# Optimization experiments

Measured on AMD Instinct MI355X. Metric: run time of the kernel, lower is better.

Reference implementation:

```python
import jax, jax.numpy as jnp
import numpy as np

B, N, DIM, H = 8, 2048, 64, 8  # per-head dim == DIM (module convention: inner_dim = dim * n_heads)


def setup_inputs() -> dict:
    key = jax.random.key(0)
    k1, k2, k3 = jax.random.split(key, 3)
    x = jax.random.normal(k1, (B, N, DIM), dtype=jnp.float32)
    W_qkv = jax.random.normal(k2, (DIM, 3 * H * DIM), dtype=jnp.float32) * (DIM ** -0.5)
    W_out = jax.random.normal(k3, (H * DIM, DIM), dtype=jnp.float32) * ((H * DIM) ** -0.5)
    b_out = jnp.zeros((DIM,), dtype=jnp.float32)
    return {"x": x, "W_qkv": W_qkv, "W_out": W_out, "b_out": b_out}


def reference(x, W_qkv, W_out, b_out):
    b, n, d = x.shape
    h = W_qkv.shape[1] // (3 * d)
    qkv = x @ W_qkv                                   # [b, n, 3*h*d]
    q, k, v = jnp.split(qkv, 3, axis=-1)              # each [b, n, h*d]
    def to_heads(t):
        return t.reshape(b, n, h, d).transpose(0, 2, 1, 3)  # [b, h, n, d]
    q, k, v = map(to_heads, (q, k, v))
    scale = d ** -0.5
    dot = jnp.einsum('bhid,bhjd->bhij', q, k) * scale  # [b, h, n, n]
    A = jax.nn.softmax(dot, axis=-1)
    z = jnp.einsum('bhij,bhjd->bhid', A, v)            # [b, h, n, d]
    z = z.transpose(0, 2, 1, 3).reshape(b, n, h * d)   # [b, n, h*d]
    return z @ W_out + b_out                           # [b, n, d]
```

## Files before the change

### kernel.cpp

```cpp
#include <hip/hip_runtime.h>
#include <math.h>

#define BB 8
#define NN 2048
#define DD 64
#define HH 8
#define BH (BB*HH)
#define HD (HH*DD)
#define NROWS (BB*NN)
#define QKV_COLS (3*HD)

typedef __bf16 bf16_8 __attribute__((ext_vector_type(8)));
typedef __bf16 bf16_4 __attribute__((ext_vector_type(4)));
typedef float  f32_16 __attribute__((ext_vector_type(16)));
typedef float  f32_4  __attribute__((ext_vector_type(4)));
typedef int    i32_2  __attribute__((ext_vector_type(2)));

__device__ __forceinline__ unsigned pack_bf16(float a, float b) {
  union { __bf16 h[2]; unsigned u; } t;
  t.h[0] = (__bf16)a; t.h[1] = (__bf16)b;
  return t.u;
}

__device__ __forceinline__ float fast_exp2(float x) {
#if __has_builtin(__builtin_amdgcn_exp2f)
  return __builtin_amdgcn_exp2f(x);
#else
  return __expf(x * 0.69314718056f);
#endif
}

__global__ __launch_bounds__(256) void wtrans_kernel(
    const float* __restrict__ Wqkv, const float* __restrict__ Wout,
    __bf16* __restrict__ Wtq, __bf16* __restrict__ Wto) {
  int idx = blockIdx.x * 256 + threadIdx.x;
  if (idx < 64 * QKV_COLS) {
    int k = idx / QKV_COLS, col = idx % QKV_COLS;
    float v = Wqkv[idx];
    if (col < HD) v *= 0.125f * 1.44269504088896f;
    Wtq[col * 64 + k] = (__bf16)v;
    (void)k;
  } else {
    int j = idx - 64 * QKV_COLS;
    int k = j >> 6, col = j & 63;
    Wto[col * 512 + k] = (__bf16)Wout[j];
  }
}

__global__ __launch_bounds__(256) void qkv_kernel(
    const float* __restrict__ x, const __bf16* __restrict__ Wtq,
    __bf16* __restrict__ Q, __bf16* __restrict__ K, __bf16* __restrict__ Vt) {
  __shared__ __bf16 T[4][64][34];
  const int lane = threadIdx.x & 63;
  const int wave = threadIdx.x >> 6;
  const int l31  = lane & 31, lhi = lane >> 5;
  const int cg   = blockIdx.x;
  const int row0 = blockIdx.y * 128 + wave * 32;

  const float* xr = x + (size_t)(row0 + l31) * 64 + lhi * 8;
  bf16_8 af[4];
#pragma unroll
  for (int s = 0; s < 4; s++) {
    f32_4 a0 = *(const f32_4*)(xr + s * 16);
    f32_4 a1 = *(const f32_4*)(xr + s * 16 + 4);
#pragma unroll
    for (int j = 0; j < 4; j++) { af[s][j] = (__bf16)a0[j]; af[s][4 + j] = (__bf16)a1[j]; }
  }

  f32_16 C0, C1;
#pragma unroll
  for (int i = 0; i < 16; i++) { C0[i] = 0.f; C1[i] = 0.f; }

  const __bf16* wb = Wtq + (size_t)cg * 64 * 64 + lhi * 8;
#pragma unroll
  for (int s = 0; s < 4; s++) {
    bf16_8 b0 = *(const bf16_8*)(wb + (size_t)l31 * 64 + s * 16);
    bf16_8 b1 = *(const bf16_8*)(wb + (size_t)(32 + l31) * 64 + s * 16);
    C0 = __builtin_amdgcn_mfma_f32_32x32x16_bf16(af[s], b0, C0, 0, 0, 0);
    C1 = __builtin_amdgcn_mfma_f32_32x32x16_bf16(af[s], b1, C1, 0, 0, 0);
  }

  const int col0  = cg * 64;
  const int which = col0 >> 9;
  const int h     = (col0 >> 6) & 7;
  const int b     = row0 >> 11;
  const int n0l   = row0 & 2047;

  if (which < 2) {
    __bf16* dst = (which == 0) ? Q : K;
#pragma unroll
    for (int r = 0; r < 16; r++) {
      int nl = (r & 3) + 8 * (r >> 2) + 4 * lhi;
      size_t base = (((size_t)(b * HH + h) * NN) + n0l + nl) * DD;
      dst[base + l31]      = (__bf16)C0[r];
      dst[base + 32 + l31] = (__bf16)C1[r];
    }
  } else {
    __bf16 (*Tw)[34] = T[wave];
#pragma unroll
    for (int r = 0; r < 16; r++) {
      int nl = (r & 3) + 8 * (r >> 2) + 4 * lhi;
      Tw[l31][nl]      = (__bf16)C0[r];
      Tw[32 + l31][nl] = (__bf16)C1[r];
    }
    __bf16* dst = Vt + (((size_t)(b * HH + h) * DD) + lane) * NN + n0l;
#pragma unroll
    for (int j = 0; j < 4; j++) {
      *(bf16_8*)(dst + j * 8) = *(const bf16_8*)(&Tw[lane][j * 8]);
    }
  }
}

__global__ __launch_bounds__(256, 3) void attn_kernel(
    const __bf16* __restrict__ Q, const __bf16* __restrict__ K,
    const __bf16* __restrict__ Vt, __bf16* __restrict__ z) {
  __shared__ __bf16 Ks[128 * 72];
  __shared__ __bf16 Vs[64 * 136];

  const int tid  = threadIdx.x;
  const int wave = tid >> 6;
  const int lane = tid & 63;
  const int l31  = lane & 31;
  const int lhi  = lane >> 5;
  const int xl   = lane ^ 32;
  const int bh   = blockIdx.x >> 4;
  const int q0   = (blockIdx.x & 15) * 128 + wave * 32;

  const __bf16* Qbase = Q + ((size_t)bh * NN + q0 + l31) * DD + lhi * 8;
  bf16_8 qf[4];
#pragma unroll
  for (int s = 0; s < 4; s++) qf[s] = *(const bf16_8*)(Qbase + s * 16);

  f32_16 O0, O1;
#pragma unroll
  for (int i = 0; i < 16; i++) { O0[i] = 0.f; O1[i] = 0.f; }
  float ls0 = 0.f, ls1 = 0.f;

  const __bf16* Kb = K  + (size_t)bh * NN * DD;
  const __bf16* Vb = Vt + (size_t)bh * DD * NN;

  const int krow = tid >> 3, kcol = (tid & 7) * 8;
  const int vrow = tid >> 4, vcol = (tid & 15) * 8;
  const __bf16* kgl = Kb + krow * 64 + kcol;
  const __bf16* vgl = Vb + (size_t)vrow * NN + vcol;
  __bf16* klds = &Ks[krow * 72 + kcol];
  __bf16* vlds = &Vs[vrow * 136 + vcol];

  bf16_8 gk[4], gv[4];
#pragma unroll
  for (int i = 0; i < 4; i++) {
    gk[i] = *(const bf16_8*)(kgl + i * 32 * 64);
    gv[i] = *(const bf16_8*)(vgl + i * 16 * NN);
  }

  for (int kt = 0; kt < NN; kt += 128) {
    __syncthreads();
#pragma unroll
    for (int i = 0; i < 4; i++) {
      *(bf16_8*)(klds + i * 32 * 72)  = gk[i];
      *(bf16_8*)(vlds + i * 16 * 136) = gv[i];
    }
    __syncthreads();
    if (kt + 128 < NN) {
#pragma unroll
      for (int i = 0; i < 4; i++) {
        gk[i] = *(const bf16_8*)(kgl + (kt + 128) * 64 + i * 32 * 64);
        gv[i] = *(const bf16_8*)(vgl + (kt + 128) + i * 16 * NN);
      }
    }

#pragma unroll
    for (int hf = 0; hf < 2; hf++) {
      f32_16 S0, S1;
#pragma unroll
      for (int i = 0; i < 16; i++) { S0[i] = 0.f; S1[i] = 0.f; }
#pragma unroll
      for (int s = 0; s < 4; s++) {
        bf16_8 kb0 = *(const bf16_8*)(&Ks[(hf * 64 + l31) * 72 + s * 16 + lhi * 8]);
        bf16_8 kb1 = *(const bf16_8*)(&Ks[(hf * 64 + 32 + l31) * 72 + s * 16 + lhi * 8]);
        S0 = __builtin_amdgcn_mfma_f32_32x32x16_bf16(kb0, qf[s], S0, 0, 0, 0);
        S1 = __builtin_amdgcn_mfma_f32_32x32x16_bf16(kb1, qf[s], S1, 0, 0, 0);
      }

      unsigned pk[16];
#pragma unroll
      for (int t = 0; t < 8; t++) {
        float a = fast_exp2(S0[2 * t]), b = fast_exp2(S0[2 * t + 1]);
        float c = fast_exp2(S1[2 * t]), d = fast_exp2(S1[2 * t + 1]);
        ls0 += a + b;
        ls1 += c + d;
        pk[t]     = pack_bf16(a, b);
        pk[8 + t] = pack_bf16(c, d);
      }

#pragma unroll
      for (int g = 0; g < 4; g++) {
        const int base = (g >> 1) * 8 + (g & 1) * 4;
        int a0 = (int)pk[base + 0], a1 = (int)pk[base + 1];
        int a2 = (int)pk[base + 2], a3 = (int)pk[base + 3];
        union { unsigned u[4]; bf16_8 v; } F;
#if __has_builtin(__builtin_amdgcn_permlane32_swap)
        i32_2 r02 = __builtin_amdgcn_permlane32_swap(a0, a2, false, false);
        i32_2 r13 = __builtin_amdgcn_permlane32_swap(a1, a3, false, false);
        F.u[0] = (unsigned)r02.x; F.u[2] = (unsigned)r02.y;
        F.u[1] = (unsigned)r13.x; F.u[3] = (unsigned)r13.y;
#else
        unsigned w0 = (unsigned)__shfl(a0, xl, 64);
        unsigned w1 = (unsigned)__shfl(a1, xl, 64);
        unsigned w2 = (unsigned)__shfl(a2, xl, 64);
        unsigned w3 = (unsigned)__shfl(a3, xl, 64);
        F.u[0] = lhi ? w2 : (unsigned)a0;
        F.u[1] = lhi ? w3 : (unsigned)a1;
        F.u[2] = lhi ? (unsigned)a2 : w0;
        F.u[3] = lhi ? (unsigned)a3 : w1;
#endif
        bf16_8 va0 = *(const bf16_8*)(&Vs[l31 * 136 + hf * 64 + g * 16 + lhi * 8]);
        bf16_8 va1 = *(const bf16_8*)(&Vs[(32 + l31) * 136 + hf * 64 + g * 16 + lhi * 8]);
        O0 = __builtin_amdgcn_mfma_f32_32x32x16_bf16(va0, F.v, O0, 0, 0, 0);
        O1 = __builtin_amdgcn_mfma_f32_32x32x16_bf16(va1, F.v, O1, 0, 0, 0);
      }
    }
  }

  float lsum = ls0 + ls1;
  lsum += __shfl_xor(lsum, 32, 64);
  const float inv = 1.f / lsum;

  __syncthreads();
  __bf16* ow = Ks + wave * (32 * 72);
#pragma unroll
  for (int g = 0; g < 4; g++) {
    bf16_4 p0, p1;
#pragma unroll
    for (int i = 0; i < 4; i++) {
      p0[i] = (__bf16)(O0[4 * g + i] * inv);
      p1[i] = (__bf16)(O1[4 * g + i] * inv);
    }
    const int d0 = 8 * g + 4 * lhi;
    *(bf16_4*)(ow + l31 * 72 + d0)      = p0;
    *(bf16_4*)(ow + l31 * 72 + 32 + d0) = p1;
  }
  const int b = bh >> 3, h = bh & 7;
  const int qr = lane >> 1, c0 = (lane & 1) * 32;
  __bf16* zp = z + ((size_t)b * NN + q0 + qr) * HD + h * DD + c0;
#pragma unroll
  for (int j = 0; j < 4; j++) {
    *(bf16_8*)(zp + 8 * j) = *(const bf16_8*)(ow + qr * 72 + c0 + 8 * j);
  }
}

__global__ __launch_bounds__(256) void out_proj_kernel(
    const __bf16* __restrict__ z, const __bf16* __restrict__ Wto,
    const float* __restrict__ bout, float* __restrict__ out) {
  __shared__ float red[2][64][36];
  const int tid  = threadIdx.x;
  const int wave = tid >> 6, lane = tid & 63;
  const int rt   = wave >> 1, kh = wave & 1;
  const int l31  = lane & 31, lhi = lane >> 5;
  const int row0 = blockIdx.x * 64 + rt * 32;

  const __bf16* zr = z   + (size_t)(row0 + l31) * HD + kh * 256 + lhi * 8;
  const __bf16* w0 = Wto + (size_t)l31 * HD        + kh * 256 + lhi * 8;
  const __bf16* w1 = Wto + (size_t)(32 + l31) * HD + kh * 256 + lhi * 8;

  f32_16 C0, C1;
#pragma unroll
  for (int i = 0; i < 16; i++) { C0[i] = 0.f; C1[i] = 0.f; }

#pragma unroll
  for (int s = 0; s < 16; s++) {
    bf16_8 a  = *(const bf16_8*)(zr + s * 16);
    bf16_8 b0 = *(const bf16_8*)(w0 + s * 16);
    bf16_8 b1 = *(const bf16_8*)(w1 + s * 16);
    C0 = __builtin_amdgcn_mfma_f32_32x32x16_bf16(a, b0, C0, 0, 0, 0);
    C1 = __builtin_amdgcn_mfma_f32_32x32x16_bf16(a, b1, C1, 0, 0, 0);
  }

  float* rw = &red[rt][lane][0];
  if (kh) {
#pragma unroll
    for (int r = 0; r < 16; r++) { rw[r] = C0[r]; rw[16 + r] = C1[r]; }
  }
  __syncthreads();
  if (!kh) {
    const float bi0 = bout[l31], bi1 = bout[32 + l31];
#pragma unroll
    for (int r = 0; r < 16; r++) {
      int n = row0 + (r & 3) + 8 * (r >> 2) + 4 * lhi;
      out[(size_t)n * 64 + l31]      = C0[r] + rw[r]      + bi0;
      out[(size_t)n * 64 + 32 + l31] = C1[r] + rw[16 + r] + bi1;
    }
  }
}

extern "C" void kernel_launch(void* const* d_in, const int* in_sizes, int n_in,
                              void* d_out, int out_size, void* d_ws, size_t ws_size,
                              hipStream_t stream) {
  const float* x    = (const float*)d_in[0];
  const float* Wqkv = (const float*)d_in[1];
  const float* Wout = (const float*)d_in[2];
  const float* bout = (const float*)d_in[3];
  float* out = (float*)d_out;

  const size_t buf_elems = (size_t)BB * HH * NN * DD;
  __bf16* Qw  = (__bf16*)d_ws;
  __bf16* Kw  = Qw  + buf_elems;
  __bf16* Vtw = Kw  + buf_elems;
  __bf16* zw  = Vtw + buf_elems;
  __bf16* Wtq = zw  + buf_elems;
  __bf16* Wto = Wtq + (size_t)QKV_COLS * 64;

  wtrans_kernel<<<512, 256, 0, stream>>>(Wqkv, Wout, Wtq, Wto);
  qkv_kernel<<<dim3(QKV_COLS / 64, NROWS / 128), 256, 0, stream>>>(x, Wtq, Qw, Kw, Vtw);
  attn_kernel<<<BH * (NN / 128), 256, 0, stream>>>(Qw, Kw, Vtw, zw);
  out_proj_kernel<<<NROWS / 64, 256, 0, stream>>>(zw, Wto, bout, out);
}
```

Before: 192.9 us.

## Fold weight prep into QKV kernel, widen attention blocks, split out-proj K four ways

Removes the separate weight-transpose kernel. The QKV kernel now reads the fp32 W_qkv directly with on-the-fly scaling and bf16 conversion, and an extra grid row packs W_out into an MFMA-friendly layout. The attention kernel moves to 512-thread blocks covering 256 queries, so each K/V tile staged in LDS is shared by twice as many waves. The output projection uses 32-row blocks with a four-way K split reduced through LDS. The cost is strided uncoalesced weight loads inside the QKV GEMM, and out_proj's read of the packed W_out now depends on writes made by an extra block row of the previous kernel on the same stream.

```diff
diff --git a/kernel.cpp b/kernel.cpp
--- a/kernel.cpp
+++ b/kernel.cpp
@@ -16,6 +16,8 @@
 typedef float  f32_4  __attribute__((ext_vector_type(4)));
 typedef int    i32_2  __attribute__((ext_vector_type(2)));
 
+#define QSCALE 0.180336880111f
+
 __device__ __forceinline__ unsigned pack_bf16(float a, float b) {
   union { __bf16 h[2]; unsigned u; } t;
   t.h[0] = (__bf16)a; t.h[1] = (__bf16)b;
@@ -30,27 +32,46 @@
 #endif
 }
 
-__global__ __launch_bounds__(256) void wtrans_kernel(
-    const float* __restrict__ Wqkv, const float* __restrict__ Wout,
-    __bf16* __restrict__ Wtq, __bf16* __restrict__ Wto) {
-  int idx = blockIdx.x * 256 + threadIdx.x;
-  if (idx < 64 * QKV_COLS) {
-    int k = idx / QKV_COLS, col = idx % QKV_COLS;
-    float v = Wqkv[idx];
-    if (col < HD) v *= 0.125f * 1.44269504088896f;
-    Wtq[col * 64 + k] = (__bf16)v;
-    (void)k;
-  } else {
-    int j = idx - 64 * QKV_COLS;
-    int k = j >> 6, col = j & 63;
-    Wto[col * 512 + k] = (__bf16)Wout[j];
-  }
+__device__ __forceinline__ bf16_8 half_swap(unsigned a0, unsigned a1,
+                                            unsigned a2, unsigned a3,
+                                            int lhi, int xl) {
+  union { unsigned u[4]; bf16_8 v; } F;
+#if __has_builtin(__builtin_amdgcn_permlane32_swap)
+  i32_2 r02 = __builtin_amdgcn_permlane32_swap((int)a0, (int)a2, false, false);
+  i32_2 r13 = __builtin_amdgcn_permlane32_swap((int)a1, (int)a3, false, false);
+  F.u[0] = (unsigned)r02.x; F.u[2] = (unsigned)r02.y;
+  F.u[1] = (unsigned)r13.x; F.u[3] = (unsigned)r13.y;
+#else
+  unsigned w0 = (unsigned)__shfl((int)a0, xl, 64);
+  unsigned w1 = (unsigned)__shfl((int)a1, xl, 64);
+  unsigned w2 = (unsigned)__shfl((int)a2, xl, 64);
+  unsigned w3 = (unsigned)__shfl((int)a3, xl, 64);
+  F.u[0] = lhi ? w2 : a0;
+  F.u[1] = lhi ? w3 : a1;
+  F.u[2] = lhi ? a2 : w0;
+  F.u[3] = lhi ? a3 : w1;
+#endif
+  return F.v;
 }
 
 __global__ __launch_bounds__(256) void qkv_kernel(
-    const float* __restrict__ x, const __bf16* __restrict__ Wtq,
-    __bf16* __restrict__ Q, __bf16* __restrict__ K, __bf16* __restrict__ Vt) {
+    const float* __restrict__ x, const float* __restrict__ Wqkv,
+    const float* __restrict__ Wout,
+    __bf16* __restrict__ Q, __bf16* __restrict__ K, __bf16* __restrict__ Vt,
+    __bf16* __restrict__ Wob) {
   __shared__ __bf16 T[4][64][34];
+
+  if (blockIdx.y == (NROWS / 128)) {
+    int id = blockIdx.x * 256 + threadIdx.x;
+    for (int e = id; e < 512 * 64; e += 24 * 256) {
+      int kf = e >> 6, col = e & 63;
+      int s = kf >> 4, lh = (kf >> 3) & 1, j = kf & 7;
+      int t = col >> 5, lc = col & 31;
+      Wob[((size_t)((t * 32 + s) * 64 + lh * 32 + lc)) * 8 + j] = (__bf16)Wout[e];
+    }
+    return;
+  }
+
   const int lane = threadIdx.x & 63;
   const int wave = threadIdx.x >> 6;
   const int l31  = lane & 31, lhi = lane >> 5;
@@ -67,24 +88,30 @@
     for (int j = 0; j < 4; j++) { af[s][j] = (__bf16)a0[j]; af[s][4 + j] = (__bf16)a1[j]; }
   }
 
+  const int col0  = cg * 64;
+  const int which = col0 >> 9;
+  const float wscl = (which == 0) ? QSCALE : 1.0f;
+
   f32_16 C0, C1;
 #pragma unroll
   for (int i = 0; i < 16; i++) { C0[i] = 0.f; C1[i] = 0.f; }
 
-  const __bf16* wb = Wtq + (size_t)cg * 64 * 64 + lhi * 8;
 #pragma unroll
   for (int s = 0; s < 4; s++) {
-    bf16_8 b0 = *(const bf16_8*)(wb + (size_t)l31 * 64 + s * 16);
-    bf16_8 b1 = *(const bf16_8*)(wb + (size_t)(32 + l31) * 64 + s * 16);
+    bf16_8 b0, b1;
+#pragma unroll
+    for (int j = 0; j < 8; j++) {
+      int k = s * 16 + lhi * 8 + j;
+      b0[j] = (__bf16)(Wqkv[(size_t)k * QKV_COLS + col0 + l31]      * wscl);
+      b1[j] = (__bf16)(Wqkv[(size_t)k * QKV_COLS + col0 + 32 + l31] * wscl);
+    }
     C0 = __builtin_amdgcn_mfma_f32_32x32x16_bf16(af[s], b0, C0, 0, 0, 0);
     C1 = __builtin_amdgcn_mfma_f32_32x32x16_bf16(af[s], b1, C1, 0, 0, 0);
   }
 
-  const int col0  = cg * 64;
-  const int which = col0 >> 9;
-  const int h     = (col0 >> 6) & 7;
-  const int b     = row0 >> 11;
-  const int n0l   = row0 & 2047;
+  const int h   = (col0 >> 6) & 7;
+  const int b   = row0 >> 11;
+  const int n0l = row0 & 2047;
 
   if (which < 2) {
     __bf16* dst = (which == 0) ? Q : K;
@@ -111,11 +138,12 @@
   }
 }
 
-__global__ __launch_bounds__(256, 3) void attn_kernel(
+__global__ __launch_bounds__(512, 4) void attn_kernel(
     const __bf16* __restrict__ Q, const __bf16* __restrict__ K,
     const __bf16* __restrict__ Vt, __bf16* __restrict__ z) {
-  __shared__ __bf16 Ks[128 * 72];
-  __shared__ __bf16 Vs[64 * 136];
+  __shared__ __bf16 SMEM[128 * 72 + 64 * 136];
+  __bf16* Ks = SMEM;
+  __bf16* Vs = SMEM + 128 * 72;
 
   const int tid  = threadIdx.x;
   const int wave = tid >> 6;
@@ -123,8 +151,8 @@
   const int l31  = lane & 31;
   const int lhi  = lane >> 5;
   const int xl   = lane ^ 32;
-  const int bh   = blockIdx.x >> 4;
-  const int q0   = (blockIdx.x & 15) * 128 + wave * 32;
+  const int bh   = blockIdx.x >> 3;
+  const int q0   = (blockIdx.x & 7) * 256 + wave * 32;
 
   const __bf16* Qbase = Q + ((size_t)bh * NN + q0 + l31) * DD + lhi * 8;
   bf16_8 qf[4];
@@ -141,31 +169,31 @@
 
   const int krow = tid >> 3, kcol = (tid & 7) * 8;
   const int vrow = tid >> 4, vcol = (tid & 15) * 8;
-  const __bf16* kgl = Kb + krow * 64 + kcol;
+  const __bf16* kgl = Kb + (size_t)krow * 64 + kcol;
   const __bf16* vgl = Vb + (size_t)vrow * NN + vcol;
   __bf16* klds = &Ks[krow * 72 + kcol];
   __bf16* vlds = &Vs[vrow * 136 + vcol];
 
-  bf16_8 gk[4], gv[4];
-#pragma unroll
-  for (int i = 0; i < 4; i++) {
-    gk[i] = *(const bf16_8*)(kgl + i * 32 * 64);
-    gv[i] = *(const bf16_8*)(vgl + i * 16 * NN);
+  bf16_8 gk[2], gv[2];
+#pragma unroll
+  for (int i = 0; i < 2; i++) {
+    gk[i] = *(const bf16_8*)(kgl + (size_t)i * 64 * 64);
+    gv[i] = *(const bf16_8*)(vgl + (size_t)i * 32 * NN);
   }
 
   for (int kt = 0; kt < NN; kt += 128) {
     __syncthreads();
 #pragma unroll
-    for (int i = 0; i < 4; i++) {
-      *(bf16_8*)(klds + i * 32 * 72)  = gk[i];
-      *(bf16_8*)(vlds + i * 16 * 136) = gv[i];
+    for (int i = 0; i < 2; i++) {
+      *(bf16_8*)(klds + i * 64 * 72)  = gk[i];
+      *(bf16_8*)(vlds + i * 32 * 136) = gv[i];
     }
     __syncthreads();
     if (kt + 128 < NN) {
 #pragma unroll
-      for (int i = 0; i < 4; i++) {
-        gk[i] = *(const bf16_8*)(kgl + (kt + 128) * 64 + i * 32 * 64);
-        gv[i] = *(const bf16_8*)(vgl + (kt + 128) + i * 16 * NN);
+      for (int i = 0; i < 2; i++) {
+        gk[i] = *(const bf16_8*)(kgl + (size_t)(kt + 128) * 64 + (size_t)i * 64 * 64);
+        gv[i] = *(const bf16_8*)(vgl + (kt + 128) + (size_t)i * 32 * NN);
       }
     }
 
@@ -196,28 +224,11 @@
 #pragma unroll
       for (int g = 0; g < 4; g++) {
         const int base = (g >> 1) * 8 + (g & 1) * 4;
-        int a0 = (int)pk[base + 0], a1 = (int)pk[base + 1];
-        int a2 = (int)pk[base + 2], a3 = (int)pk[base + 3];
-        union { unsigned u[4]; bf16_8 v; } F;
-#if __has_builtin(__builtin_amdgcn_permlane32_swap)
-        i32_2 r02 = __builtin_amdgcn_permlane32_swap(a0, a2, false, false);
-        i32_2 r13 = __builtin_amdgcn_permlane32_swap(a1, a3, false, false);
-        F.u[0] = (unsigned)r02.x; F.u[2] = (unsigned)r02.y;
-        F.u[1] = (unsigned)r13.x; F.u[3] = (unsigned)r13.y;
-#else
-        unsigned w0 = (unsigned)__shfl(a0, xl, 64);
-        unsigned w1 = (unsigned)__shfl(a1, xl, 64);
-        unsigned w2 = (unsigned)__shfl(a2, xl, 64);
-        unsigned w3 = (unsigned)__shfl(a3, xl, 64);
-        F.u[0] = lhi ? w2 : (unsigned)a0;
-        F.u[1] = lhi ? w3 : (unsigned)a1;
-        F.u[2] = lhi ? (unsigned)a2 : w0;
-        F.u[3] = lhi ? (unsigned)a3 : w1;
-#endif
+        bf16_8 F = half_swap(pk[base], pk[base + 1], pk[base + 2], pk[base + 3], lhi, xl);
         bf16_8 va0 = *(const bf16_8*)(&Vs[l31 * 136 + hf * 64 + g * 16 + lhi * 8]);
         bf16_8 va1 = *(const bf16_8*)(&Vs[(32 + l31) * 136 + hf * 64 + g * 16 + lhi * 8]);
-        O0 = __builtin_amdgcn_mfma_f32_32x32x16_bf16(va0, F.v, O0, 0, 0, 0);
-        O1 = __builtin_amdgcn_mfma_f32_32x32x16_bf16(va1, F.v, O1, 0, 0, 0);
+        O0 = __builtin_amdgcn_mfma_f32_32x32x16_bf16(va0, F, O0, 0, 0, 0);
+        O1 = __builtin_amdgcn_mfma_f32_32x32x16_bf16(va1, F, O1, 0, 0, 0);
       }
     }
   }
@@ -227,7 +238,7 @@
   const float inv = 1.f / lsum;
 
   __syncthreads();
-  __bf16* ow = Ks + wave * (32 * 72);
+  __bf16* ow = SMEM + wave * (32 * 68);
 #pragma unroll
   for (int g = 0; g < 4; g++) {
     bf16_4 p0, p1;
@@ -237,58 +248,58 @@
       p1[i] = (__bf16)(O1[4 * g + i] * inv);
     }
     const int d0 = 8 * g + 4 * lhi;
-    *(bf16_4*)(ow + l31 * 72 + d0)      = p0;
-    *(bf16_4*)(ow + l31 * 72 + 32 + d0) = p1;
+    *(bf16_4*)(ow + l31 * 68 + d0)      = p0;
+    *(bf16_4*)(ow + l31 * 68 + 32 + d0) = p1;
   }
   const int b = bh >> 3, h = bh & 7;
   const int qr = lane >> 1, c0 = (lane & 1) * 32;
   __bf16* zp = z + ((size_t)b * NN + q0 + qr) * HD + h * DD + c0;
 #pragma unroll
   for (int j = 0; j < 4; j++) {
-    *(bf16_8*)(zp + 8 * j) = *(const bf16_8*)(ow + qr * 72 + c0 + 8 * j);
+    *(bf16_8*)(zp + 8 * j) = *(const bf16_8*)(ow + qr * 68 + c0 + 8 * j);
   }
 }
 
 __global__ __launch_bounds__(256) void out_proj_kernel(
-    const __bf16* __restrict__ z, const __bf16* __restrict__ Wto,
+    const __bf16* __restrict__ z, const __bf16* __restrict__ Wob,
     const float* __restrict__ bout, float* __restrict__ out) {
-  __shared__ float red[2][64][36];
+  __shared__ float red[3][64][33];
   const int tid  = threadIdx.x;
   const int wave = tid >> 6, lane = tid & 63;
-  const int rt   = wave >> 1, kh = wave & 1;
   const int l31  = lane & 31, lhi = lane >> 5;
-  const int row0 = blockIdx.x * 64 + rt * 32;
-
-  const __bf16* zr = z   + (size_t)(row0 + l31) * HD + kh * 256 + lhi * 8;
-  const __bf16* w0 = Wto + (size_t)l31 * HD        + kh * 256 + lhi * 8;
-  const __bf16* w1 = Wto + (size_t)(32 + l31) * HD + kh * 256 + lhi * 8;
+  const int row0 = blockIdx.x * 32;
+
+  const __bf16* zr = z + (size_t)(row0 + l31) * HD + wave * 128 + lhi * 8;
 
   f32_16 C0, C1;
 #pragma unroll
   for (int i = 0; i < 16; i++) { C0[i] = 0.f; C1[i] = 0.f; }
 
 #pragma unroll
-  for (int s = 0; s < 16; s++) {
+  for (int s = 0; s < 8; s++) {
+    const int sa = wave * 8 + s;
     bf16_8 a  = *(const bf16_8*)(zr + s * 16);
-    bf16_8 b0 = *(const bf16_8*)(w0 + s * 16);
-    bf16_8 b1 = *(const bf16_8*)(w1 + s * 16);
+    bf16_8 b0 = *(const bf16_8*)(Wob + ((size_t)((0 * 32 + sa) * 64 + lane)) * 8);
+    bf16_8 b1 = *(const bf16_8*)(Wob + ((size_t)((1 * 32 + sa) * 64 + lane)) * 8);
     C0 = __builtin_amdgcn_mfma_f32_32x32x16_bf16(a, b0, C0, 0, 0, 0);
     C1 = __builtin_amdgcn_mfma_f32_32x32x16_bf16(a, b1, C1, 0, 0, 0);
   }
 
-  float* rw = &red[rt][lane][0];
-  if (kh) {
+  if (wave) {
+    float* rw = &red[wave - 1][lane][0];
 #pragma unroll
     for (int r = 0; r < 16; r++) { rw[r] = C0[r]; rw[16 + r] = C1[r]; }
   }
   __syncthreads();
-  if (!kh) {
+  if (wave == 0) {
     const float bi0 = bout[l31], bi1 = bout[32 + l31];
 #pragma unroll
     for (int r = 0; r < 16; r++) {
       int n = row0 + (r & 3) + 8 * (r >> 2) + 4 * lhi;
-      out[(size_t)n * 64 + l31]      = C0[r] + rw[r]      + bi0;
-      out[(size_t)n * 64 + 32 + l31] = C1[r] + rw[16 + r] + bi1;
+      float v0 = C0[r] + red[0][lane][r]      + red[1][lane][r]      + red[2][lane][r];
+      float v1 = C1[r] + red[0][lane][16 + r] + red[1][lane][16 + r] + red[2][lane][16 + r];
+      out[(size_t)n * 64 + l31]      = v0 + bi0;
+      out[(size_t)n * 64 + 32 + l31] = v1 + bi1;
     }
   }
 }
@@ -307,11 +318,10 @@
   __bf16* Kw  = Qw  + buf_elems;
   __bf16* Vtw = Kw  + buf_elems;
   __bf16* zw  = Vtw + buf_elems;
-  __bf16* Wtq = zw  + buf_elems;
-  __bf16* Wto = Wtq + (size_t)QKV_COLS * 64;
-
-  wtrans_kernel<<<512, 256, 0, stream>>>(Wqkv, Wout, Wtq, Wto);
-  qkv_kernel<<<dim3(QKV_COLS / 64, NROWS / 128), 256, 0, stream>>>(x, Wtq, Qw, Kw, Vtw);
-  attn_kernel<<<BH * (NN / 128), 256, 0, stream>>>(Qw, Kw, Vtw, zw);
-  out_proj_kernel<<<NROWS / 64, 256, 0, stream>>>(zw, Wto, bout, out);
-}
+  __bf16* Wob = zw  + buf_elems;
+
+  qkv_kernel<<<dim3(QKV_COLS / 64, NROWS / 128 + 1), 256, 0, stream>>>(
+      x, Wqkv, Wout, Qw, Kw, Vtw, Wob);
+  attn_kernel<<<BH * (NN / 256), 512, 0, stream>>>(Qw, Kw, Vtw, zw);
+  out_proj_kernel<<<NROWS / 32, 256, 0, stream>>>(zw, Wob, bout, out);
+}
```

Measured after the change: 220.4 us. 14.3% more time.
